# Kernel tuning notes

Hardware: AMD Instinct MI355X
Metric: run time of the kernel (lower is better)

## Reference

```python
import jax, jax.numpy as jnp
import numpy as np

N, B, NPG, E = 16384, 64, 256, 524288
F_IN, POS_DIM, L_PE = 32, 3, 8
W, HEADS, LAYERS, DFF = 256, 8, 2, 1024
HID, OUT = 512, 64
S = NPG + 1
DH = W // HEADS


def _ln(x, s, b, eps=1e-5):
    m = jnp.mean(x, -1, keepdims=True)
    v = jnp.var(x, -1, keepdims=True)
    return (x - m) * jax.lax.rsqrt(v + eps) * s + b


def _gelu(x):
    # custom tanh-approx GELU from the source module
    c = float(np.sqrt(2.0 / np.pi))
    return 0.5 * x * (1.0 + jnp.tanh(c * (x + 0.044715 * x ** 3)))


def setup_inputs() -> dict:
    key = jax.random.key(0)
    ks = jax.random.split(key, 24)
    nrm = lambda k, shape, s=0.05: jax.random.normal(k, shape, jnp.float32) * s
    D_IN = F_IN + POS_DIM * L_PE  # 56
    inp = {}
    inp['x'] = jax.random.normal(ks[0], (N, F_IN), jnp.float32)
    inp['p'] = jax.random.uniform(ks[1], (N, POS_DIM), jnp.float32, -1.0, 1.0)
    inp['edge_index'] = jax.random.randint(ks[2], (2, E), 0, N, jnp.int32)
    inp['batch'] = (jnp.arange(N) // NPG).astype(jnp.int32)  # sorted, 64 equal graphs
    inp['gcn_w'] = nrm(ks[3], (D_IN, W), 0.1)
    inp['gcn_b'] = jnp.zeros((W,), jnp.float32)
    inp['cls_token'] = nrm(ks[4], (1, 1, W), 0.02)
    inp['ln_pre_s'] = jnp.ones((W,), jnp.float32)
    inp['ln_pre_b'] = jnp.zeros((W,), jnp.float32)
    inp['norm1_s'] = jnp.ones((LAYERS, W), jnp.float32)
    inp['norm1_b'] = jnp.zeros((LAYERS, W), jnp.float32)
    inp['in_proj_w'] = nrm(ks[5], (LAYERS, W, 3 * W))
    inp['in_proj_b'] = jnp.zeros((LAYERS, 3 * W), jnp.float32)
    inp['out_proj_w'] = nrm(ks[6], (LAYERS, W, W))
    inp['out_proj_b'] = jnp.zeros((LAYERS, W), jnp.float32)
    inp['norm2_s'] = jnp.ones((LAYERS, W), jnp.float32)
    inp['norm2_b'] = jnp.zeros((LAYERS, W), jnp.float32)
    inp['ff_w1'] = nrm(ks[7], (LAYERS, W, DFF))
    inp['ff_b1'] = jnp.zeros((LAYERS, DFF), jnp.float32)
    inp['ff_w2'] = nrm(ks[8], (LAYERS, DFF, W))
    inp['ff_b2'] = jnp.zeros((LAYERS, W), jnp.float32)
    inp['ln_post_s'] = jnp.ones((W,), jnp.float32)
    inp['ln_post_b'] = jnp.zeros((W,), jnp.float32)
    inp['dec_w1'] = nrm(ks[9], (W, HID))
    inp['dec_b1'] = jnp.zeros((HID,), jnp.float32)
    inp['dec_w2'] = nrm(ks[10], (HID, HID))
    inp['dec_b2'] = jnp.zeros((HID,), jnp.float32)
    inp['dec_w3'] = nrm(ks[11], (HID, OUT))
    inp['dec_b3'] = jnp.zeros((OUT,), jnp.float32)
    return inp


def _forward(x, p, gcn_w, gcn_b, cls_token, ln_pre_s, ln_pre_b, norm1_s, norm1_b,
             in_proj_w, in_proj_b, out_proj_w, out_proj_b, norm2_s, norm2_b,
             ff_w1, ff_b1, ff_w2, ff_b2, ln_post_s, ln_post_b,
             dec_w1, dec_b1, dec_w2, dec_b2, dec_w3, dec_b3, edge_index, batch):
    # positional encoding: sin(p * 2^i * pi), i = 0..L-1
    freqs = (2.0 ** jnp.arange(L_PE, dtype=jnp.float32)) * jnp.pi
    pe = jnp.sin(p[:, :, None] * freqs).reshape(N, POS_DIM * L_PE)
    xc = jnp.concatenate([x, pe], axis=-1)  # [N, 56]
    # GCNConv: x W, then sym-normalized aggregation with self loops, + bias
    xw = xc @ gcn_w  # [N, W]
    loop = jnp.arange(N, dtype=edge_index.dtype)
    row = jnp.concatenate([edge_index[0], loop])
    col = jnp.concatenate([edge_index[1], loop])
    deg = jax.ops.segment_sum(jnp.ones_like(row, dtype=xw.dtype), col, num_segments=N)
    dinv = jax.lax.rsqrt(jnp.maximum(deg, 1e-12))
    coef = dinv[row] * dinv[col]
    h = jax.ops.segment_sum(coef[:, None] * xw[row], col, num_segments=N) + gcn_b
    # to_dense_batch (batch is sorted graph ids)
    counts = jax.ops.segment_sum(jnp.ones((N,), jnp.int32), batch, num_segments=B)
    ptr = jnp.concatenate([jnp.zeros((1,), jnp.int32), jnp.cumsum(counts)[:-1]])
    pos = jnp.arange(N, dtype=jnp.int32) - ptr[batch]
    dense = jnp.zeros((B, NPG, W), h.dtype).at[batch, pos].set(h)
    mask = jnp.zeros((B, NPG), bool).at[batch, pos].set(True)
    # prepend cls token
    xd = jnp.concatenate([jnp.broadcast_to(cls_token, (B, 1, W)), dense], axis=1)  # [B,S,W]
    valid = jnp.concatenate([jnp.ones((B, 1), bool), mask], axis=1)  # [B,S]
    xd = _ln(xd, ln_pre_s, ln_pre_b)
    # causal mask with row 0 (cls) unmasked
    am = jnp.triu(jnp.ones((S, S), bool), k=1)
    am = am.at[0, :].set(False)
    allowed = (~am)[None, :, :] & valid[:, None, :]  # [B,S,S]
    scale = 1.0 / float(np.sqrt(DH))
    for l in range(LAYERS):
        h1 = _ln(xd, norm1_s[l], norm1_b[l])
        qkv = h1 @ in_proj_w[l] + in_proj_b[l]  # [B,S,3W]
        q, k, v = jnp.split(qkv, 3, axis=-1)
        q = q.reshape(B, S, HEADS, DH)
        k = k.reshape(B, S, HEADS, DH)
        v = v.reshape(B, S, HEADS, DH)
        sc = jnp.einsum('bqhd,bkhd->bhqk', q, k) * scale
        sc = jnp.where(allowed[:, None, :, :], sc, -1e9)
        a = jax.nn.softmax(sc, axis=-1)
        o = jnp.einsum('bhqk,bkhd->bqhd', a, v).reshape(B, S, W)
        xd = xd + (o @ out_proj_w[l] + out_proj_b[l])
        h2 = _ln(xd, norm2_s[l], norm2_b[l])
        # MLP(num_layers=2) applies activation after BOTH layers (incl. last)
        ff = _gelu(_gelu(h2 @ ff_w1[l] + ff_b1[l]) @ ff_w2[l] + ff_b2[l])
        xd = xd + ff
    cls = _ln(xd[:, 0, :], ln_post_s, ln_post_b)
    # decoder MLP(num_layers=3) with relu after every layer (incl. last)
    h3 = jax.nn.relu(cls @ dec_w1 + dec_b1)
    h3 = jax.nn.relu(h3 @ dec_w2 + dec_b2)
    return jax.nn.relu(h3 @ dec_w3 + dec_b3)


def reference(x, p, gcn_w, gcn_b, cls_token, ln_pre_s, ln_pre_b, norm1_s, norm1_b,
              in_proj_w, in_proj_b, out_proj_w, out_proj_b, norm2_s, norm2_b,
              ff_w1, ff_b1, ff_w2, ff_b2, ln_post_s, ln_post_b,
              dec_w1, dec_b1, dec_w2, dec_b2, dec_w3, dec_b3, edge_index, batch):
    return _forward(x, p, gcn_w, gcn_b, cls_token, ln_pre_s, ln_pre_b, norm1_s, norm1_b,
                    in_proj_w, in_proj_b, out_proj_w, out_proj_b, norm2_s, norm2_b,
                    ff_w1, ff_b1, ff_w2, ff_b2, ln_post_s, ln_post_b,
                    dec_w1, dec_b1, dec_w2, dec_b2, dec_w3, dec_b3, edge_index, batch)
```

## Files before the change

### kernel.cpp

```cpp
#include <hip/hip_runtime.h>
#include <math.h>

constexpr int N_NODES = 16384;
constexpr int BGRAPH  = 64;
constexpr int NEDGE   = 524288;
constexpr int SEQ     = 257;
constexpr int WDIM    = 256;
constexpr int DFF     = 1024;
constexpr int HID     = 512;
constexpr int MROWS   = BGRAPH * SEQ;

constexpr size_t F_Y    = 0;
constexpr size_t F_AGG  = F_Y    + (size_t)N_NODES * 64;
constexpr size_t F_XD   = F_AGG  + (size_t)N_NODES * 64;
constexpr size_t F_CLS  = F_XD   + (size_t)MROWS * WDIM;
constexpr size_t F_D1   = F_CLS  + (size_t)BGRAPH * WDIM;
constexpr size_t F_D2   = F_D1   + (size_t)BGRAPH * HID;
constexpr size_t F_WPAD = F_D2   + (size_t)BGRAPH * HID;
constexpr size_t F_DINV = F_WPAD + (size_t)64 * WDIM;
constexpr size_t F_IEND = F_DINV + (size_t)N_NODES;

typedef __attribute__((ext_vector_type(8))) __bf16 bf16x8;
typedef __attribute__((ext_vector_type(4))) __bf16 bf16x4;
typedef __attribute__((ext_vector_type(4))) float f32x4;

__device__ __forceinline__ float gelu_f(float x) {
    float u = 0.7978845608028654f * (x + 0.044715f * x * x * x);
    return 0.5f * x * (1.0f + tanhf(u));
}

__global__ __launch_bounds__(256) void hist_kernel(const int* __restrict__ col, int* __restrict__ indeg) {
    int e = blockIdx.x * 256 + threadIdx.x;
    atomicAdd(&indeg[col[e]], 1);
}

__global__ __launch_bounds__(1024) void scan_kernel(const int* __restrict__ indeg, int* __restrict__ offs,
                                                    int* __restrict__ cursor, float* __restrict__ dinv) {
    __shared__ int parts[1024];
    int t = threadIdx.x;
    int base = t * 16;
    int loc[16];
    int s = 0;
#pragma unroll
    for (int i = 0; i < 16; ++i) { loc[i] = indeg[base + i]; s += loc[i]; }
    parts[t] = s;
    __syncthreads();
    for (int off = 1; off < 1024; off <<= 1) {
        int v = (t >= off) ? parts[t - off] : 0;
        __syncthreads();
        parts[t] += v;
        __syncthreads();
    }
    int run = (t == 0) ? 0 : parts[t - 1];
#pragma unroll
    for (int i = 0; i < 16; ++i) {
        offs[base + i] = run;
        cursor[base + i] = run;
        dinv[base + i] = rsqrtf((float)loc[i] + 1.0f);
        run += loc[i];
    }
    if (t == 1023) offs[N_NODES] = run;
}

__global__ __launch_bounds__(256) void fill_kernel(const int* __restrict__ ei, int* __restrict__ cursor,
                                                   int* __restrict__ csr) {
    int e = blockIdx.x * 256 + threadIdx.x;
    int r = ei[e];
    int c = ei[NEDGE + e];
    int pos = atomicAdd(&cursor[c], 1);
    csr[pos] = r;
}

__global__ __launch_bounds__(256) void y_kernel(const float* __restrict__ x, const float* __restrict__ p,
                                                const float* __restrict__ dinv, float* __restrict__ y) {
    int idx = blockIdx.x * 256 + threadIdx.x;
    int i = idx >> 6, d = idx & 63;
    float v = 0.f;
    if (d < 32) {
        v = x[i * 32 + d];
    } else if (d < 56) {
        int dd = d - 32;
        int dim = dd >> 3, j = dd & 7;
        v = sinf(p[i * 3 + dim] * (3.14159265358979323846f * (float)(1 << j)));
    }
    y[idx] = dinv[i] * v;
}

__global__ __launch_bounds__(256) void agg_kernel(const float* __restrict__ y, const float* __restrict__ dinv,
                                                  const int* __restrict__ offs, const int* __restrict__ csr,
                                                  float* __restrict__ agg) {
    int c = (blockIdx.x * 256 + threadIdx.x) >> 6;
    int lane = threadIdx.x & 63;
    float acc = y[(size_t)c * 64 + lane];
    int s = offs[c], e = offs[c + 1];
    for (int j = s; j < e; ++j) {
        int r = csr[j];
        acc += y[(size_t)r * 64 + lane];
    }
    agg[(size_t)c * 64 + lane] = dinv[c] * acc;
}

__global__ __launch_bounds__(256) void wpad_kernel(const float* __restrict__ w, float* __restrict__ wp) {
    int idx = blockIdx.x * 256 + threadIdx.x;
    wp[idx] = (idx < 56 * 256) ? w[idx] : 0.f;
}

__global__ __launch_bounds__(256) void cls_write(const float* __restrict__ tok, float* __restrict__ xd) {
    xd[(size_t)blockIdx.x * SEQ * WDIM + threadIdx.x] = tok[threadIdx.x];
}

template <int OUTBF>
__global__ __launch_bounds__(256) void ln4_kernel(const float* __restrict__ in, int rin_stride,
                                                  void* __restrict__ out,
                                                  const float* __restrict__ g, const float* __restrict__ be) {
    int w = threadIdx.x >> 6, lane = threadIdx.x & 63;
    int row = blockIdx.x * 4 + w;
    const float* ip = in + (size_t)row * rin_stride + lane * 4;
    f32x4 v = *(const f32x4*)ip;
    float s = v[0] + v[1] + v[2] + v[3];
    float ss = v[0] * v[0] + v[1] * v[1] + v[2] * v[2] + v[3] * v[3];
#pragma unroll
    for (int off = 1; off < 64; off <<= 1) { s += __shfl_xor(s, off); ss += __shfl_xor(ss, off); }
    float mean = s * 0.00390625f;
    float var = ss * 0.00390625f - mean * mean;
    float rs = rsqrtf(var + 1e-5f);
    f32x4 gv = *(const f32x4*)(g + lane * 4);
    f32x4 bv = *(const f32x4*)(be + lane * 4);
    if (OUTBF) {
        bf16x4 o;
#pragma unroll
        for (int i = 0; i < 4; ++i) o[i] = (__bf16)((v[i] - mean) * rs * gv[i] + bv[i]);
        *(bf16x4*)((__bf16*)out + (size_t)row * 256 + lane * 4) = o;
    } else {
        f32x4 o;
#pragma unroll
        for (int i = 0; i < 4; ++i) o[i] = (v[i] - mean) * rs * gv[i] + bv[i];
        *(f32x4*)((float*)out + (size_t)row * 256 + lane * 4) = o;
    }
}

__global__ __launch_bounds__(256) void tcast_kernel(const float* __restrict__ W, __bf16* __restrict__ Wt,
                                                    int K, int N) {
    __shared__ __bf16 T[64][65];
    int t = threadIdx.x;
    int k0 = blockIdx.x << 6, n0 = blockIdx.y << 6;
#pragma unroll
    for (int i = 0; i < 16; ++i) {
        int idx = t + i * 256;
        int k = idx >> 6, n = idx & 63;
        T[k][n] = (__bf16)W[(size_t)(k0 + k) * N + n0 + n];
    }
    __syncthreads();
#pragma unroll
    for (int i = 0; i < 16; ++i) {
        int idx = t + i * 256;
        int n = idx >> 6, k = idx & 63;
        Wt[(size_t)(n0 + n) * K + k0 + k] = T[k][n];
    }
}

constexpr int LP = 36;
template <int BN, int ACT, int OMODE>
__global__ __launch_bounds__(256) void gemm_bf(const __bf16* __restrict__ A, int lda,
                                               const __bf16* __restrict__ Bt,
                                               const float* __restrict__ bias,
                                               void* __restrict__ Cv, int ldc,
                                               int Ktot, int Mrows) {
    constexpr int NTW = BN / 32;
    __shared__ __bf16 As[128 * LP];
    __shared__ __bf16 Bs[BN * LP];
    int t = threadIdx.x;
    int m0 = blockIdx.x << 7, n0 = blockIdx.y * BN;
    int w = t >> 6, L = t & 63;
    int wm = w >> 1, wn = w & 1;
    int lc = L & 15, quad = L >> 4;

    int sa_row = t >> 1, sa_off = (t & 1) << 4;
    const __bf16* ap = A + (size_t)(m0 + sa_row) * lda + sa_off;
    __bf16* as_dst = &As[sa_row * LP + sa_off];
    const __bf16* bp;
    __bf16* bs_dst;
    if constexpr (BN == 128) {
        bp = Bt + (size_t)(n0 + sa_row) * Ktot + sa_off;
        bs_dst = &Bs[sa_row * LP + sa_off];
    } else {
        int sb_row = t >> 2, sb_off = (t & 3) << 3;
        bp = Bt + (size_t)(n0 + sb_row) * Ktot + sb_off;
        bs_dst = &Bs[sb_row * LP + sb_off];
    }

    int a_base = (wm * 64 + lc) * LP + quad * 8;
    int b_base = (wn * (BN / 2) + lc) * LP + quad * 8;

    f32x4 acc[4][NTW] = {};

    for (int k0 = 0; k0 < Ktot; k0 += 32) {
        bf16x8 a0 = *(const bf16x8*)(ap + k0);
        bf16x8 a1 = *(const bf16x8*)(ap + k0 + 8);
        bf16x8 b0, b1;
        if constexpr (BN == 128) {
            b0 = *(const bf16x8*)(bp + k0);
            b1 = *(const bf16x8*)(bp + k0 + 8);
        } else {
            b0 = *(const bf16x8*)(bp + k0);
        }
        __syncthreads();
        *(bf16x8*)as_dst = a0;
        *(bf16x8*)(as_dst + 8) = a1;
        if constexpr (BN == 128) {
            *(bf16x8*)bs_dst = b0;
            *(bf16x8*)(bs_dst + 8) = b1;
        } else {
            *(bf16x8*)bs_dst = b0;
        }
        __syncthreads();
        bf16x8 af[4], bfr[NTW];
#pragma unroll
        for (int i = 0; i < 4; ++i) af[i] = *(const bf16x8*)&As[a_base + i * 16 * LP];
#pragma unroll
        for (int i = 0; i < NTW; ++i) bfr[i] = *(const bf16x8*)&Bs[b_base + i * 16 * LP];
#pragma unroll
        for (int mt = 0; mt < 4; ++mt)
#pragma unroll
            for (int nt = 0; nt < NTW; ++nt)
                acc[mt][nt] = __builtin_amdgcn_mfma_f32_16x16x32_bf16(af[mt], bfr[nt], acc[mt][nt], 0, 0, 0);
    }

#pragma unroll
    for (int mt = 0; mt < 4; ++mt) {
        int gmb = m0 + wm * 64 + mt * 16 + quad * 4;
#pragma unroll
        for (int nt = 0; nt < NTW; ++nt) {
            int gn = n0 + wn * (BN / 2) + nt * 16 + lc;
            float bv = bias[gn];
#pragma unroll
            for (int r = 0; r < 4; ++r) {
                int gm = gmb + r;
                if (gm >= Mrows) continue;
                float v = acc[mt][nt][r] + bv;
                if (ACT == 1) v = gelu_f(v);
                if (OMODE == 0) {
                    ((__bf16*)Cv)[(size_t)gm * ldc + gn] = (__bf16)v;
                } else {
                    float* cp = (float*)Cv + (size_t)gm * ldc + gn;
                    *cp = v + *cp;
                }
            }
        }
    }
}

constexpr int PPITCH = 280;
__global__ __launch_bounds__(256, 2) void attn_mfma(const __bf16* __restrict__ qkvb,
                                                    __bf16* __restrict__ obuf) {
    __shared__ __bf16 Vt[32][PPITCH];
    __shared__ __bf16 Pb[4][16][PPITCH];
    int bb = blockIdx.x;
    int b = bb >> 3, h = bb & 7;
    int t = threadIdx.x;
    int w = t >> 6, L = t & 63;
    int c = L & 15, quad = L >> 4;
    const float scale = 0.17677669529663687f;
    const __bf16* qb = qkvb + (size_t)(b * SEQ) * 768 + h * 32;
    const __bf16* kb = qb + 256;
    const __bf16* vb = qb + 512;
    __bf16* ob = obuf + (size_t)(b * SEQ) * 256 + h * 32;

    for (int idx = t; idx < 272 * 4; idx += 256) {
        int key = idx >> 2, dc = (idx & 3) * 8;
        bf16x8 vv = {};
        if (key < SEQ) vv = *(const bf16x8*)(vb + (size_t)key * 768 + dc);
#pragma unroll
        for (int j = 0; j < 8; ++j) Vt[dc + j][key] = vv[j];
    }
    __syncthreads();

#pragma unroll 1
    for (int qt = 0; qt < 5; ++qt) {
        int q0 = qt * 64 + w * 16;
        if (q0 > 256) continue;
        int ntiles = (qt == 0 && w == 0) ? 17 : (qt * 4 + w + 1);
        if (ntiles > 17) ntiles = 17;
        int nkc = (ntiles + 1) >> 1;

        bf16x8 qf;
        {
            int qr = q0 + c; if (qr > 256) qr = 256;
            qf = *(const bf16x8*)(qb + (size_t)qr * 768 + quad * 8);
        }

        f32x4 acc[17];
#pragma unroll
        for (int tt = 0; tt < 17; ++tt) {
            if (tt >= ntiles) continue;
            int kr = tt * 16 + c; if (kr > 256) kr = 256;
            bf16x8 kf = *(const bf16x8*)(kb + (size_t)kr * 768 + quad * 8);
            f32x4 z = {0.f, 0.f, 0.f, 0.f};
            acc[tt] = __builtin_amdgcn_mfma_f32_16x16x32_bf16(qf, kf, z, 0, 0, 0);
        }

        float inv[4];
#pragma unroll
        for (int j = 0; j < 4; ++j) {
            int q = q0 + quad * 4 + j;
            float mx = -3.0e38f;
#pragma unroll
            for (int tt = 0; tt < 17; ++tt) {
                if (tt >= ntiles) continue;
                int key = tt * 16 + c;
                bool ok = (key < SEQ) && (q == 0 || key <= q);
                float v = ok ? acc[tt][j] * scale : -3.0e38f;
                mx = fmaxf(mx, v);
            }
            mx = fmaxf(mx, __shfl_xor(mx, 1));
            mx = fmaxf(mx, __shfl_xor(mx, 2));
            mx = fmaxf(mx, __shfl_xor(mx, 4));
            mx = fmaxf(mx, __shfl_xor(mx, 8));
            float s = 0.f;
#pragma unroll
            for (int tt = 0; tt < 17; ++tt) {
                if (tt >= ntiles) continue;
                int key = tt * 16 + c;
                bool ok = (key < SEQ) && (q == 0 || key <= q);
                float pv = ok ? expf(acc[tt][j] * scale - mx) : 0.f;
                s += pv;
                Pb[w][quad * 4 + j][key] = (__bf16)pv;
            }
            if ((ntiles & 1) && ntiles < 17)
                Pb[w][quad * 4 + j][ntiles * 16 + c] = (__bf16)0.f;
            s += __shfl_xor(s, 1);
            s += __shfl_xor(s, 2);
            s += __shfl_xor(s, 4);
            s += __shfl_xor(s, 8);
            inv[j] = 1.0f / s;
        }

        f32x4 oacc0 = {0.f, 0.f, 0.f, 0.f};
        f32x4 oacc1 = {0.f, 0.f, 0.f, 0.f};
#pragma unroll
        for (int kc = 0; kc < 9; ++kc) {
            if (kc >= nkc) continue;
            int off = kc * 32 + quad * 8;
            bf16x8 af = {};
            bf16x8 bf0 = {};
            bf16x8 bf1 = {};
            if (off < 257) {
                af  = *(const bf16x8*)&Pb[w][c][off];
                bf0 = *(const bf16x8*)&Vt[c][off];
                bf1 = *(const bf16x8*)&Vt[16 + c][off];
            }
            oacc0 = __builtin_amdgcn_mfma_f32_16x16x32_bf16(af, bf0, oacc0, 0, 0, 0);
            oacc1 = __builtin_amdgcn_mfma_f32_16x16x32_bf16(af, bf1, oacc1, 0, 0, 0);
        }

#pragma unroll
        for (int j = 0; j < 4; ++j) {
            int q = q0 + quad * 4 + j;
            if (q < SEQ) {
                __bf16* op = ob + (size_t)q * 256;
                op[c]      = (__bf16)(oacc0[j] * inv[j]);
                op[16 + c] = (__bf16)(oacc1[j] * inv[j]);
            }
        }
    }
}

template <int ACT, bool RESID, bool REMAP>
__global__ __launch_bounds__(256) void gemm_std(const float* __restrict__ A, int lda,
                                                const float* __restrict__ Bw, int ldb,
                                                const float* __restrict__ bias,
                                                float* __restrict__ C, int ldc, int Ktot) {
    int t = threadIdx.x;
    int m0 = blockIdx.x << 6, n0 = blockIdx.y << 6;
    __shared__ float As[16][68];
    __shared__ float Bs[16][64];
    int arow = t >> 2, akk = (t & 3) << 2;
    int bk = t >> 4, bn = (t & 15) << 2;
    int tm = (t >> 4) << 2, tn = (t & 15) << 2;
    float acc[4][4] = {};
    const float* ap = A + (size_t)(m0 + arow) * lda + akk;
    const float* bp = Bw + (size_t)bk * ldb + n0 + bn;
    for (int k0 = 0; k0 < Ktot; k0 += 16) {
        float4 av = *(const float4*)(ap + k0);
        float4 bv = *(const float4*)(bp + (size_t)k0 * ldb);
        __syncthreads();
        As[akk + 0][arow] = av.x; As[akk + 1][arow] = av.y;
        As[akk + 2][arow] = av.z; As[akk + 3][arow] = av.w;
        *(float4*)&Bs[bk][bn] = bv;
        __syncthreads();
#pragma unroll
        for (int k = 0; k < 16; ++k) {
            float4 a = *(const float4*)&As[k][tm];
            float4 b = *(const float4*)&Bs[k][tn];
            acc[0][0] += a.x * b.x; acc[0][1] += a.x * b.y; acc[0][2] += a.x * b.z; acc[0][3] += a.x * b.w;
            acc[1][0] += a.y * b.x; acc[1][1] += a.y * b.y; acc[1][2] += a.y * b.z; acc[1][3] += a.y * b.w;
            acc[2][0] += a.z * b.x; acc[2][1] += a.z * b.y; acc[2][2] += a.z * b.z; acc[2][3] += a.z * b.w;
            acc[3][0] += a.w * b.x; acc[3][1] += a.w * b.y; acc[3][2] += a.w * b.z; acc[3][3] += a.w * b.w;
        }
    }
#pragma unroll
    for (int i = 0; i < 4; ++i) {
        int gm = m0 + tm + i;
        int orow = REMAP ? (gm + (gm >> 8) + 1) : gm;
        float* cp = C + (size_t)orow * ldc + n0 + tn;
        float4 r;
        r.x = acc[i][0] + bias[n0 + tn + 0];
        r.y = acc[i][1] + bias[n0 + tn + 1];
        r.z = acc[i][2] + bias[n0 + tn + 2];
        r.w = acc[i][3] + bias[n0 + tn + 3];
        if (ACT == 1) { r.x = gelu_f(r.x); r.y = gelu_f(r.y); r.z = gelu_f(r.z); r.w = gelu_f(r.w); }
        if (ACT == 2) { r.x = fmaxf(r.x, 0.f); r.y = fmaxf(r.y, 0.f); r.z = fmaxf(r.z, 0.f); r.w = fmaxf(r.w, 0.f); }
        if (RESID) {
            float4 o = *(const float4*)cp;
            r.x += o.x; r.y += o.y; r.z += o.z; r.w += o.w;
        }
        *(float4*)cp = r;
    }
}

template <int K, int NOUT>
__global__ __launch_bounds__(256) void dec_fc2(const float* __restrict__ in, const float* __restrict__ w,
                                               const float* __restrict__ bia, float* __restrict__ out) {
    __shared__ float rowbuf[K];
    __shared__ float part[4][64];
    int b = blockIdx.x, c = blockIdx.y, t = threadIdx.x;
    for (int i = t; i < K; i += 256) rowbuf[i] = in[(size_t)b * K + i];
    __syncthreads();
    int lane = t & 63, wv = t >> 6;
    int n = c * 64 + lane;
    const int KQ = K / 4;
    const float* wp = w + (size_t)(wv * KQ) * NOUT + n;
    float s = 0.f;
#pragma unroll 8
    for (int k = 0; k < KQ; ++k) s += rowbuf[wv * KQ + k] * wp[(size_t)k * NOUT];
    part[wv][lane] = s;
    __syncthreads();
    if (wv == 0) {
        float r = part[0][lane] + part[1][lane] + part[2][lane] + part[3][lane] + bia[n];
        out[(size_t)b * NOUT + n] = fmaxf(r, 0.f);
    }
}

extern "C" void kernel_launch(void* const* d_in, const int* in_sizes, int n_in,
                              void* d_out, int out_size, void* d_ws, size_t ws_size,
                              hipStream_t stream) {
    const float* x         = (const float*)d_in[0];
    const float* p         = (const float*)d_in[1];
    const int*   ei        = (const int*)d_in[2];
    const float* gcn_w     = (const float*)d_in[4];
    const float* gcn_b     = (const float*)d_in[5];
    const float* cls_tok   = (const float*)d_in[6];
    const float* ln_pre_s  = (const float*)d_in[7];
    const float* ln_pre_b  = (const float*)d_in[8];
    const float* norm1_s   = (const float*)d_in[9];
    const float* norm1_b   = (const float*)d_in[10];
    const float* in_proj_w = (const float*)d_in[11];
    const float* in_proj_b = (const float*)d_in[12];
    const float* out_proj_w= (const float*)d_in[13];
    const float* out_proj_b= (const float*)d_in[14];
    const float* norm2_s   = (const float*)d_in[15];
    const float* norm2_b   = (const float*)d_in[16];
    const float* ff_w1     = (const float*)d_in[17];
    const float* ff_b1     = (const float*)d_in[18];
    const float* ff_w2     = (const float*)d_in[19];
    const float* ff_b2     = (const float*)d_in[20];
    const float* ln_post_s = (const float*)d_in[21];
    const float* ln_post_b = (const float*)d_in[22];
    const float* dec_w1    = (const float*)d_in[23];
    const float* dec_b1    = (const float*)d_in[24];
    const float* dec_w2    = (const float*)d_in[25];
    const float* dec_b2    = (const float*)d_in[26];
    const float* dec_w3    = (const float*)d_in[27];
    const float* dec_b3    = (const float*)d_in[28];

    float* ws   = (float*)d_ws;
    float* y    = ws + F_Y;
    float* agg  = ws + F_AGG;
    float* xd   = ws + F_XD;
    float* cls  = ws + F_CLS;
    float* dd1  = ws + F_D1;
    float* dd2  = ws + F_D2;
    float* wpad = ws + F_WPAD;
    float* dinv = ws + F_DINV;
    int* ibase  = (int*)(ws + F_IEND);
    int* indeg  = ibase;
    int* offs   = ibase + N_NODES;
    int* cursor = offs + N_NODES + 1;
    int* csr    = cursor + N_NODES;
    uintptr_t ub = ((uintptr_t)(csr + NEDGE) + 15) & ~(uintptr_t)15;
    __bf16* h1b  = (__bf16*)ub;
    __bf16* qkvb = h1b  + (size_t)MROWS * 256;
    __bf16* ffbb = qkvb + (size_t)MROWS * 768;
    __bf16* wt_in  = ffbb  + (size_t)MROWS * 1024;
    __bf16* wt_out = wt_in  + 2 * 768 * 256;
    __bf16* wt_f1  = wt_out + 2 * 256 * 256;
    __bf16* wt_f2  = wt_f1  + 2 * 1024 * 256;

    hipMemsetAsync(indeg, 0, N_NODES * sizeof(int), stream);
    hist_kernel<<<NEDGE / 256, 256, 0, stream>>>(ei + NEDGE, indeg);
    scan_kernel<<<1, 1024, 0, stream>>>(indeg, offs, cursor, dinv);
    fill_kernel<<<NEDGE / 256, 256, 0, stream>>>(ei, cursor, csr);
    y_kernel<<<N_NODES * 64 / 256, 256, 0, stream>>>(x, p, dinv, y);
    agg_kernel<<<N_NODES / 4, 256, 0, stream>>>(y, dinv, offs, csr, agg);
    wpad_kernel<<<64, 256, 0, stream>>>(gcn_w, wpad);

    for (int l = 0; l < 2; ++l) {
        tcast_kernel<<<dim3(4, 12), 256, 0, stream>>>(in_proj_w + (size_t)l * 256 * 768,
                                                      wt_in + (size_t)l * 768 * 256, 256, 768);
        tcast_kernel<<<dim3(4, 4), 256, 0, stream>>>(out_proj_w + (size_t)l * 256 * 256,
                                                     wt_out + (size_t)l * 256 * 256, 256, 256);
        tcast_kernel<<<dim3(4, 16), 256, 0, stream>>>(ff_w1 + (size_t)l * 256 * 1024,
                                                      wt_f1 + (size_t)l * 1024 * 256, 256, 1024);
        tcast_kernel<<<dim3(16, 4), 256, 0, stream>>>(ff_w2 + (size_t)l * 1024 * 256,
                                                      wt_f2 + (size_t)l * 256 * 1024, 1024, 256);
    }

    gemm_std<0, false, true><<<dim3(256, 4), 256, 0, stream>>>(agg, 64, wpad, 256, gcn_b, xd, 256, 64);
    cls_write<<<64, 256, 0, stream>>>(cls_tok, xd);
    ln4_kernel<0><<<MROWS / 4, 256, 0, stream>>>(xd, 256, xd, ln_pre_s, ln_pre_b);

    const int MB = (MROWS + 127) / 128;
    for (int l = 0; l < 2; ++l) {
        ln4_kernel<1><<<MROWS / 4, 256, 0, stream>>>(xd, 256, h1b, norm1_s + l * WDIM, norm1_b + l * WDIM);
        gemm_bf<128, 0, 0><<<dim3(MB, 6), 256, 0, stream>>>(
            h1b, 256, wt_in + (size_t)l * 768 * 256, in_proj_b + l * 768, qkvb, 768, 256, MROWS);
        attn_mfma<<<512, 256, 0, stream>>>(qkvb, h1b);
        gemm_bf<64, 0, 1><<<dim3(MB, 4), 256, 0, stream>>>(
            h1b, 256, wt_out + (size_t)l * 256 * 256, out_proj_b + l * WDIM, xd, 256, 256, MROWS);
        ln4_kernel<1><<<MROWS / 4, 256, 0, stream>>>(xd, 256, h1b, norm2_s + l * WDIM, norm2_b + l * WDIM);
        gemm_bf<128, 1, 0><<<dim3(MB, 8), 256, 0, stream>>>(
            h1b, 256, wt_f1 + (size_t)l * 1024 * 256, ff_b1 + l * DFF, ffbb, 1024, 256, MROWS);
        gemm_bf<64, 1, 1><<<dim3(MB, 4), 256, 0, stream>>>(
            ffbb, 1024, wt_f2 + (size_t)l * 256 * 1024, ff_b2 + l * WDIM, xd, 256, 1024, MROWS);
    }

    ln4_kernel<0><<<BGRAPH / 4, 256, 0, stream>>>(xd, SEQ * WDIM, cls, ln_post_s, ln_post_b);
    dec_fc2<256, 512><<<dim3(BGRAPH, 8), 256, 0, stream>>>(cls, dec_w1, dec_b1, dd1);
    dec_fc2<512, 512><<<dim3(BGRAPH, 8), 256, 0, stream>>>(dd1, dec_w2, dec_b2, dd2);
    dec_fc2<512, 64><<<dim3(BGRAPH, 1), 256, 0, stream>>>(dd2, dec_w3, dec_b3, (float*)d_out);
}
```

Before: 786.3 us.

## Prefetch next K-tile into registers and group-swizzle GEMM block order

```diff
diff --git a/kernel.cpp b/kernel.cpp
--- a/kernel.cpp
+++ b/kernel.cpp
@@ -165,12 +165,20 @@
                                                const __bf16* __restrict__ Bt,
                                                const float* __restrict__ bias,
                                                void* __restrict__ Cv, int ldc,
-                                               int Ktot, int Mrows) {
+                                               int Ktot, int Mrows, int MBlocks, int NY) {
     constexpr int NTW = BN / 32;
     __shared__ __bf16 As[128 * LP];
     __shared__ __bf16 Bs[BN * LP];
+    int f = blockIdx.x;
+    int m8 = f & 7;
+    int rest = f >> 3;
+    int mg = rest / NY;
+    int yb = rest - mg * NY;
+    int mb = mg * 8 + m8;
+    if (mb >= MBlocks) return;
+    int m0 = mb << 7, n0 = yb * BN;
+
     int t = threadIdx.x;
-    int m0 = blockIdx.x << 7, n0 = blockIdx.y * BN;
     int w = t >> 6, L = t & 63;
     int wm = w >> 1, wn = w & 1;
     int lc = L & 15, quad = L >> 4;
@@ -194,16 +202,17 @@
 
     f32x4 acc[4][NTW] = {};
 
+    bf16x8 a0 = *(const bf16x8*)(ap);
+    bf16x8 a1 = *(const bf16x8*)(ap + 8);
+    bf16x8 b0, b1;
+    if constexpr (BN == 128) {
+        b0 = *(const bf16x8*)(bp);
+        b1 = *(const bf16x8*)(bp + 8);
+    } else {
+        b0 = *(const bf16x8*)(bp);
+    }
+
     for (int k0 = 0; k0 < Ktot; k0 += 32) {
-        bf16x8 a0 = *(const bf16x8*)(ap + k0);
-        bf16x8 a1 = *(const bf16x8*)(ap + k0 + 8);
-        bf16x8 b0, b1;
-        if constexpr (BN == 128) {
-            b0 = *(const bf16x8*)(bp + k0);
-            b1 = *(const bf16x8*)(bp + k0 + 8);
-        } else {
-            b0 = *(const bf16x8*)(bp + k0);
-        }
         __syncthreads();
         *(bf16x8*)as_dst = a0;
         *(bf16x8*)(as_dst + 8) = a1;
@@ -214,6 +223,16 @@
             *(bf16x8*)bs_dst = b0;
         }
         __syncthreads();
+        if (k0 + 32 < Ktot) {
+            a0 = *(const bf16x8*)(ap + k0 + 32);
+            a1 = *(const bf16x8*)(ap + k0 + 40);
+            if constexpr (BN == 128) {
+                b0 = *(const bf16x8*)(bp + k0 + 32);
+                b1 = *(const bf16x8*)(bp + k0 + 40);
+            } else {
+                b0 = *(const bf16x8*)(bp + k0 + 32);
+            }
+        }
         bf16x8 af[4], bfr[NTW];
 #pragma unroll
         for (int i = 0; i < 4; ++i) af[i] = *(const bf16x8*)&As[a_base + i * 16 * LP];
@@ -520,18 +539,19 @@
     ln4_kernel<0><<<MROWS / 4, 256, 0, stream>>>(xd, 256, xd, ln_pre_s, ln_pre_b);
 
     const int MB = (MROWS + 127) / 128;
+    const int MG8 = (MB + 7) / 8;
     for (int l = 0; l < 2; ++l) {
         ln4_kernel<1><<<MROWS / 4, 256, 0, stream>>>(xd, 256, h1b, norm1_s + l * WDIM, norm1_b + l * WDIM);
-        gemm_bf<128, 0, 0><<<dim3(MB, 6), 256, 0, stream>>>(
-            h1b, 256, wt_in + (size_t)l * 768 * 256, in_proj_b + l * 768, qkvb, 768, 256, MROWS);
+        gemm_bf<128, 0, 0><<<8 * 6 * MG8, 256, 0, stream>>>(
+            h1b, 256, wt_in + (size_t)l * 768 * 256, in_proj_b + l * 768, qkvb, 768, 256, MROWS, MB, 6);
         attn_mfma<<<512, 256, 0, stream>>>(qkvb, h1b);
-        gemm_bf<64, 0, 1><<<dim3(MB, 4), 256, 0, stream>>>(
-            h1b, 256, wt_out + (size_t)l * 256 * 256, out_proj_b + l * WDIM, xd, 256, 256, MROWS);
+        gemm_bf<64, 0, 1><<<8 * 4 * MG8, 256, 0, stream>>>(
+            h1b, 256, wt_out + (size_t)l * 256 * 256, out_proj_b + l * WDIM, xd, 256, 256, MROWS, MB, 4);
         ln4_kernel<1><<<MROWS / 4, 256, 0, stream>>>(xd, 256, h1b, norm2_s + l * WDIM, norm2_b + l * WDIM);
-        gemm_bf<128, 1, 0><<<dim3(MB, 8), 256, 0, stream>>>(
-            h1b, 256, wt_f1 + (size_t)l * 1024 * 256, ff_b1 + l * DFF, ffbb, 1024, 256, MROWS);
-        gemm_bf<64, 1, 1><<<dim3(MB, 4), 256, 0, stream>>>(
-            ffbb, 1024, wt_f2 + (size_t)l * 256 * 1024, ff_b2 + l * WDIM, xd, 256, 1024, MROWS);
+        gemm_bf<128, 1, 0><<<8 * 8 * MG8, 256, 0, stream>>>(
+            h1b, 256, wt_f1 + (size_t)l * 1024 * 256, ff_b1 + l * DFF, ffbb, 1024, 256, MROWS, MB, 8);
+        gemm_bf<64, 1, 1><<<8 * 4 * MG8, 256, 0, stream>>>(
+            ffbb, 1024, wt_f2 + (size_t)l * 256 * 1024, ff_b2 + l * WDIM, xd, 256, 1024, MROWS, MB, 4);
     }
 
     ln4_kernel<0><<<BGRAPH / 4, 256, 0, stream>>>(xd, SEQ * WDIM, cls, ln_post_s, ln_post_b);
```

Measured after the change: 741.5 us. -5.7%, faster.
